# Optimization experiments

Hardware: AMD Instinct MI355X
Metric: run time of the kernel (lower is better)

The kernel has to match this reference:

```python
import jax, jax.numpy as jnp
import numpy as np
from jax import lax

R = 4                 # radius (init kwarg)
EPS = 2.0             # eps (init kwarg)
K = 2 * R + 1         # stencil size


def _dir_kernels():
    """8 directional box kernels [8,1,K,K]: L,R,U,D,NW,NE,SW,SE (matches torch construction)."""
    base = np.ones((K, K), np.float32)
    L = base.copy(); L[:, R + 1:] = 0
    Rk = base.copy(); Rk[:, :R] = 0
    U = base.copy(); U[R + 1:, :] = 0
    D = base.copy(); D[:R, :] = 0
    NW = U.copy(); NE = U.copy(); SW = D.copy(); SE = D.copy()
    half = float((R + 1) * (2 * R + 1))
    L, Rk, U, D = L / half, Rk / half, U / half, D / half
    NW[:, R + 1:] = 0; NE[:, :R] = 0; SW[:, R + 1:] = 0; SE[:, :R] = 0
    quad = float((R + 1) ** 2)
    NW, NE, SW, SE = NW / quad, NE / quad, SW / quad, SE / quad
    return jnp.asarray(np.stack([L, Rk, U, D, NW, NE, SW, SE])[:, None])


def _pad(x):
    # ReplicationPad2d(R)
    return jnp.pad(x, ((0, 0), (0, 0), (R, R), (R, R)), mode='edge')


def _conv(x, w, groups=1):
    return lax.conv_general_dilated(
        x, w, window_strides=(1, 1), padding='VALID',
        dimension_numbers=('NCHW', 'OIHW', 'NCHW'), feature_group_count=groups)


def _resize_bilinear_ac(x, H, W):
    """Bilinear resize with align_corners=True, separable gather. x: [N,C,h,w]."""
    n, c, h, w = x.shape
    dt = x.dtype

    def coords(out, src):
        t = jnp.arange(out, dtype=dt) * (jnp.asarray(src - 1, dt) / jnp.asarray(out - 1, dt))
        i0 = jnp.clip(jnp.floor(t).astype(jnp.int32), 0, src - 2)
        f = t - i0.astype(dt)
        return i0, f

    y0, fy = coords(H, h)
    x0, fx = coords(W, w)
    rows = x[:, :, y0, :] * (1 - fy)[None, None, :, None] + x[:, :, y0 + 1, :] * fy[None, None, :, None]
    return rows[:, :, :, x0] * (1 - fx) + rows[:, :, :, x0 + 1] * fx


def setup_inputs() -> dict:
    key = jax.random.key(0)
    k1, k2, k3 = jax.random.split(key, 3)
    lr_x = jax.random.uniform(k1, (1, 3, 256, 256), jnp.float32) * 255.0
    lr_y = jax.random.uniform(k2, (1, 3, 256, 256), jnp.float32) * 255.0
    hr_x = jax.random.uniform(k3, (1, 3, 1024, 1024), jnp.float32) * 255.0
    box_w = jnp.full((3, 1, K, K), 1.0 / (K * K), jnp.float32)  # depthwise box filter weights
    return {"lr_x": lr_x, "lr_y": lr_y, "hr_x": hr_x, "box_w": box_w}


def reference(lr_x, lr_y, hr_x, box_w):
    H, W = hr_x.shape[2], hr_x.shape[3]
    box = lambda t: _conv(_pad(t), box_w, groups=3)

    # --- guided filter coefficients at low res ---
    mean_x = box(lr_x)
    mean_y = box(lr_y)
    cov_xy = box(lr_x * lr_y) - mean_x * mean_y
    var_x = box(lr_x * lr_x) - mean_x * mean_x
    A = cov_xy / (var_x + EPS)
    b = mean_y - A * mean_x

    # --- upsample A, b to hr (bilinear, align_corners=True) ---
    A = _resize_bilinear_ac(A, H, W)
    b = _resize_bilinear_ac(b, H, W)

    # --- 8-direction side-window stencil; channels treated as batch ---
    dirw = _dir_kernels()                      # [8,1,K,K]
    A3 = _pad(A.reshape(3, 1, H, W))
    b3 = _pad(b.reshape(3, 1, H, W))
    im3 = hr_x.reshape(3, 1, H, W)
    cA = _conv(A3, dirw)                       # [3,8,H,W]
    cB = _conv(b3, dirw)                       # [3,8,H,W]
    d = cA * im3 + cB - im3                    # [3,8,H,W]

    idx = jnp.argmin(jnp.abs(d), axis=1, keepdims=True)
    dm = jnp.take_along_axis(d, idx, axis=1)   # min-|delta| direction
    res = (dm + im3).reshape(1, 3, H, W)

    # res.int() truncates toward zero, then clamp(0,255), then float
    return jnp.clip(jnp.trunc(res), 0.0, 255.0)
```

## Files before the change

kernel.cpp:

```cpp
#include <hip/hip_runtime.h>

#define RR 4
#define LRN 256
#define HRN 1024
#define SCALE (255.0f/1023.0f)

#define LTW 32
#define LTH 8
#define LGW (LTW + 2*RR)
#define LGH (LTH + 2*RR)

#define TX 32
#define TYR 64
#define BTH 8
#define NROW (TYR / BTH)
#define LRC 12
#define LRR 20

__global__ __launch_bounds__(256) void lowres_coeffs(
    const float* __restrict__ lrx, const float* __restrict__ lry,
    float2* __restrict__ AB)
{
    __shared__ float4 sV[LGH][LGW];
    __shared__ float4 sH[LGH][LTW];

    const int c  = blockIdx.z;
    const int X0 = blockIdx.x * LTW, Y0 = blockIdx.y * LTH;
    const int tid = threadIdx.y * LTW + threadIdx.x;
    const float* px = lrx + c * LRN * LRN;
    const float* py = lry + c * LRN * LRN;

    for (int i = tid; i < LGH * LGW; i += 256) {
        int r = i / LGW, col = i - r * LGW;
        int gy = min(max(Y0 - RR + r, 0), LRN - 1);
        int gx = min(max(X0 - RR + col, 0), LRN - 1);
        float xv = px[gy * LRN + gx];
        float yv = py[gy * LRN + gx];
        sV[r][col] = make_float4(xv, yv, xv * yv, xv * xv);
    }
    __syncthreads();

    for (int i = tid; i < LGH * LTW; i += 256) {
        int r = i / LTW, col = i - r * LTW;
        float4 s = sV[r][col];
        #pragma unroll
        for (int k = 1; k < 9; ++k) {
            float4 v = sV[r][col + k];
            s.x += v.x; s.y += v.y; s.z += v.z; s.w += v.w;
        }
        sH[r][col] = s;
    }
    __syncthreads();

    const int tx = threadIdx.x, ty = threadIdx.y;
    float4 s = sH[ty][tx];
    #pragma unroll
    for (int k = 1; k < 9; ++k) {
        float4 v = sH[ty + k][tx];
        s.x += v.x; s.y += v.y; s.z += v.z; s.w += v.w;
    }
    const float inv81 = 1.0f / 81.0f;
    float mx = s.x * inv81, my = s.y * inv81;
    float cov = s.z * inv81 - mx * my;
    float var = s.w * inv81 - mx * mx;
    float A = cov / (var + 2.0f);
    float B = my - A * mx;
    AB[(c * LRN + Y0 + ty) * LRN + X0 + tx] = make_float2(A, B);
}

__device__ inline int anchor_of(int u) {
    int k = min(max(u - 4, 0), HRN - 1);
    float t = (float)k * SCALE;
    int i = (int)t; if (i > LRN - 2) i = LRN - 2;
    return i;
}

__device__ inline float4 mkw(int k0, int k1, int a) {
    float4 w = make_float4(0.f, 0.f, 0.f, 0.f);
    for (int k = k0; k <= k1; ++k) {
        int kc = min(max(k, 0), HRN - 1);
        float t = (float)kc * SCALE;
        int i = (int)t; if (i > LRN - 2) i = LRN - 2;
        float f = t - (float)i;
        int off = i - a;
        float wa = 1.0f - f, wb = f;
        w.x += (off == 0) ? wa : 0.0f;
        w.y += (off == 1) ? wa : ((off == 0) ? wb : 0.0f);
        w.z += (off == 2) ? wa : ((off == 1) ? wb : 0.0f);
        w.w += (off == 2) ? wb : 0.0f;
    }
    return w;
}

__global__ __launch_bounds__(256, 6) void stencil_kernel(
    const float2* __restrict__ AB,
    const float* __restrict__ hrx, float* __restrict__ out)
{
    __shared__ float2 sAB[LRR][LRC];
    __shared__ float2 sT[TYR][LRC];
    __shared__ float2 sB[TYR][LRC];
    __shared__ float2 sF[TYR][LRC];
    __shared__ float4 sYW[TYR][3];
    __shared__ int    sYA[TYR];
    __shared__ float4 sXW[TX][3];
    __shared__ int    sXA[TX];

    const int c  = blockIdx.z;
    const int X0 = blockIdx.x * TX, Y0 = blockIdx.y * TYR;
    const int tid = threadIdx.y * TX + threadIdx.x;
    const float2* ABc = AB + c * LRN * LRN;

    const int rowbase = anchor_of(Y0);
    const int colbase = anchor_of(X0);

    if (tid < TX) {
        int x = X0 + tid;
        int a = anchor_of(x);
        sXA[tid] = a - colbase;
        sXW[tid][0] = mkw(x - 4, x,     a);
        sXW[tid][1] = mkw(x,     x + 4, a);
        sXW[tid][2] = mkw(x - 4, x + 4, a);
    } else if (tid >= 64 && tid < 64 + TYR) {
        int r = tid - 64;
        int y = Y0 + r;
        int a = anchor_of(y);
        sYA[r] = a - rowbase;
        sYW[r][0] = mkw(y - 4, y,     a);
        sYW[r][1] = mkw(y,     y + 4, a);
        sYW[r][2] = mkw(y - 4, y + 4, a);
    }
    for (int i = tid; i < LRR * LRC; i += 256) {
        int r = i / LRC, cc = i - r * LRC;
        int gr = min(rowbase + r, LRN - 1);
        int gc = min(colbase + cc, LRN - 1);
        sAB[r][cc] = ABc[gr * LRN + gc];
    }
    __syncthreads();

    for (int i = tid; i < TYR * LRC; i += 256) {
        int r = i / LRC, cc = i - r * LRC;
        int ra = sYA[r];
        float4 wT = sYW[r][0], wB = sYW[r][1], wF = sYW[r][2];
        float2 v0 = sAB[ra][cc],     v1 = sAB[ra + 1][cc];
        float2 v2 = sAB[ra + 2][cc], v3 = sAB[ra + 3][cc];
        sT[r][cc] = make_float2(wT.x*v0.x + wT.y*v1.x + wT.z*v2.x + wT.w*v3.x,
                                wT.x*v0.y + wT.y*v1.y + wT.z*v2.y + wT.w*v3.y);
        sB[r][cc] = make_float2(wB.x*v0.x + wB.y*v1.x + wB.z*v2.x + wB.w*v3.x,
                                wB.x*v0.y + wB.y*v1.y + wB.z*v2.y + wB.w*v3.y);
        sF[r][cc] = make_float2(wF.x*v0.x + wF.y*v1.x + wF.z*v2.x + wF.w*v3.x,
                                wF.x*v0.y + wF.y*v1.y + wF.z*v2.y + wF.w*v3.y);
    }
    __syncthreads();

    const int tx = threadIdx.x, tyw = threadIdx.y;
    const int c0 = sXA[tx];
    const float4 wL = sXW[tx][0], wR = sXW[tx][1], wFh = sXW[tx][2];
    const float i45 = 1.0f / 45.0f, i25 = 1.0f / 25.0f;
    const float* hp = hrx + (c * HRN + Y0 + tyw) * HRN + X0 + tx;
    float*       op = out + (c * HRN + Y0 + tyw) * HRN + X0 + tx;

    #pragma unroll
    for (int j = 0; j < NROW; ++j) {
        const int r = tyw + j * BTH;
        float LA=0,Lb=0, RA=0,Rb=0, UA=0,Ub=0, DA=0,Db=0;
        float NWA=0,NWb=0, NEA=0,NEb=0, SWA=0,SWb=0, SEA=0,SEb=0;
        #pragma unroll
        for (int k = 0; k < 4; ++k) {
            float wl = (k==0)?wL.x:(k==1)?wL.y:(k==2)?wL.z:wL.w;
            float wr = (k==0)?wR.x:(k==1)?wR.y:(k==2)?wR.z:wR.w;
            float wf = (k==0)?wFh.x:(k==1)?wFh.y:(k==2)?wFh.z:wFh.w;
            float2 tv = sT[r][c0 + k];
            float2 bv = sB[r][c0 + k];
            float2 fv = sF[r][c0 + k];
            LA = fmaf(wl, fv.x, LA);   Lb = fmaf(wl, fv.y, Lb);
            RA = fmaf(wr, fv.x, RA);   Rb = fmaf(wr, fv.y, Rb);
            UA = fmaf(wf, tv.x, UA);   Ub = fmaf(wf, tv.y, Ub);
            DA = fmaf(wf, bv.x, DA);   Db = fmaf(wf, bv.y, Db);
            NWA = fmaf(wl, tv.x, NWA); NWb = fmaf(wl, tv.y, NWb);
            NEA = fmaf(wr, tv.x, NEA); NEb = fmaf(wr, tv.y, NEb);
            SWA = fmaf(wl, bv.x, SWA); SWb = fmaf(wl, bv.y, SWb);
            SEA = fmaf(wr, bv.x, SEA); SEb = fmaf(wr, bv.y, SEb);
        }
        float xv = hp[j * BTH * HRN];

        float d0 = fmaf(i45, fmaf(LA,  xv, Lb),  -xv);
        float d1 = fmaf(i45, fmaf(RA,  xv, Rb),  -xv);
        float d2 = fmaf(i45, fmaf(UA,  xv, Ub),  -xv);
        float d3 = fmaf(i45, fmaf(DA,  xv, Db),  -xv);
        float d4 = fmaf(i25, fmaf(NWA, xv, NWb), -xv);
        float d5 = fmaf(i25, fmaf(NEA, xv, NEb), -xv);
        float d6 = fmaf(i25, fmaf(SWA, xv, SWb), -xv);
        float d7 = fmaf(i25, fmaf(SEA, xv, SEb), -xv);

        float a0 = fabsf(d0), a1 = fabsf(d1), a2 = fabsf(d2), a3 = fabsf(d3);
        float a4 = fabsf(d4), a5 = fabsf(d5), a6 = fabsf(d6), a7 = fabsf(d7);
        bool c01 = a0 <= a1; float w01 = c01 ? d0 : d1; float m01 = c01 ? a0 : a1;
        bool c23 = a2 <= a3; float w23 = c23 ? d2 : d3; float m23 = c23 ? a2 : a3;
        bool c45 = a4 <= a5; float w45 = c45 ? d4 : d5; float m45 = c45 ? a4 : a5;
        bool c67 = a6 <= a7; float w67 = c67 ? d6 : d7; float m67 = c67 ? a6 : a7;
        bool cA_ = m01 <= m23; float wA = cA_ ? w01 : w23; float mA = cA_ ? m01 : m23;
        bool cB_ = m45 <= m67; float wB_ = cB_ ? w45 : w67; float mB = cB_ ? m45 : m67;
        float bd = (mA <= mB) ? wA : wB_;

        float res = __builtin_amdgcn_fmed3f(truncf(bd + xv), 0.0f, 255.0f);
        op[j * BTH * HRN] = res;
    }
}

extern "C" void kernel_launch(void* const* d_in, const int* in_sizes, int n_in,
                              void* d_out, int out_size, void* d_ws, size_t ws_size,
                              hipStream_t stream) {
    const float* lrx = (const float*)d_in[0];
    const float* lry = (const float*)d_in[1];
    const float* hrx = (const float*)d_in[2];
    (void)d_in[3]; (void)in_sizes; (void)n_in; (void)out_size; (void)ws_size;

    float2* AB = (float2*)d_ws;
    float* outp = (float*)d_out;

    dim3 lblock(LTW, LTH);
    dim3 lgrid(LRN / LTW, LRN / LTH, 3);
    lowres_coeffs<<<lgrid, lblock, 0, stream>>>(lrx, lry, AB);

    dim3 sblock(TX, BTH);
    dim3 sgrid(HRN / TX, HRN / TYR, 3);
    stencil_kernel<<<sgrid, sblock, 0, stream>>>(AB, hrx, outp);
}
```

Before: 87.74 us.

## Fuse low-res guided-filter coefficient computation into the high-res stencil kernel

Removes the separate low-res coefficient kernel and its global A/B workspace; each stencil block now recomputes the box-filtered A,b for its own low-res halo tile in shared memory, reusing one shared region for both the box sums and the row-interpolated buffers. Inner accumulations are rewritten with 2-wide vector FMAs so the compiler can emit packed FP32 math. This saves one kernel launch and a global round-trip, but adds redundant halo work per block and a larger shared footprint that may reduce occupancy.

After: 85.23 us. -2.9%, faster.

```diff
diff --git a/kernel.cpp b/kernel.cpp
--- a/kernel.cpp
+++ b/kernel.cpp
@@ -4,11 +4,6 @@
 #define LRN 256
 #define HRN 1024
 #define SCALE (255.0f/1023.0f)
-
-#define LTW 32
-#define LTH 8
-#define LGW (LTW + 2*RR)
-#define LGH (LTH + 2*RR)
 
 #define TX 32
 #define TYR 64
@@ -16,57 +11,10 @@
 #define NROW (TYR / BTH)
 #define LRC 12
 #define LRR 20
-
-__global__ __launch_bounds__(256) void lowres_coeffs(
-    const float* __restrict__ lrx, const float* __restrict__ lry,
-    float2* __restrict__ AB)
-{
-    __shared__ float4 sV[LGH][LGW];
-    __shared__ float4 sH[LGH][LTW];
-
-    const int c  = blockIdx.z;
-    const int X0 = blockIdx.x * LTW, Y0 = blockIdx.y * LTH;
-    const int tid = threadIdx.y * LTW + threadIdx.x;
-    const float* px = lrx + c * LRN * LRN;
-    const float* py = lry + c * LRN * LRN;
-
-    for (int i = tid; i < LGH * LGW; i += 256) {
-        int r = i / LGW, col = i - r * LGW;
-        int gy = min(max(Y0 - RR + r, 0), LRN - 1);
-        int gx = min(max(X0 - RR + col, 0), LRN - 1);
-        float xv = px[gy * LRN + gx];
-        float yv = py[gy * LRN + gx];
-        sV[r][col] = make_float4(xv, yv, xv * yv, xv * xv);
-    }
-    __syncthreads();
-
-    for (int i = tid; i < LGH * LTW; i += 256) {
-        int r = i / LTW, col = i - r * LTW;
-        float4 s = sV[r][col];
-        #pragma unroll
-        for (int k = 1; k < 9; ++k) {
-            float4 v = sV[r][col + k];
-            s.x += v.x; s.y += v.y; s.z += v.z; s.w += v.w;
-        }
-        sH[r][col] = s;
-    }
-    __syncthreads();
-
-    const int tx = threadIdx.x, ty = threadIdx.y;
-    float4 s = sH[ty][tx];
-    #pragma unroll
-    for (int k = 1; k < 9; ++k) {
-        float4 v = sH[ty + k][tx];
-        s.x += v.x; s.y += v.y; s.z += v.z; s.w += v.w;
-    }
-    const float inv81 = 1.0f / 81.0f;
-    float mx = s.x * inv81, my = s.y * inv81;
-    float cov = s.z * inv81 - mx * my;
-    float var = s.w * inv81 - mx * mx;
-    float A = cov / (var + 2.0f);
-    float B = my - A * mx;
-    AB[(c * LRN + Y0 + ty) * LRN + X0 + tx] = make_float2(A, B);
-}
+#define GC (LRC + 8)
+#define GR (LRR + 8)
+
+typedef float v2 __attribute__((ext_vector_type(2)));
 
 __device__ inline int anchor_of(int u) {
     int k = min(max(u - 4, 0), HRN - 1);
@@ -92,14 +40,18 @@
     return w;
 }
 
-__global__ __launch_bounds__(256, 6) void stencil_kernel(
-    const float2* __restrict__ AB,
+__global__ __launch_bounds__(256, 6) void fused_kernel(
+    const float* __restrict__ lrx, const float* __restrict__ lry,
     const float* __restrict__ hrx, float* __restrict__ out)
 {
-    __shared__ float2 sAB[LRR][LRC];
-    __shared__ float2 sT[TYR][LRC];
-    __shared__ float2 sB[TYR][LRC];
-    __shared__ float2 sF[TYR][LRC];
+    __shared__ alignas(16) char region1[18432];
+    float4 (*sV)[GC]  = reinterpret_cast<float4(*)[GC]>(region1);
+    float4 (*sHS)[LRC] = reinterpret_cast<float4(*)[LRC]>(region1 + GR * GC * 16);
+    v2 (*sT)[LRC]  = reinterpret_cast<v2(*)[LRC]>(region1);
+    v2 (*sBm)[LRC] = reinterpret_cast<v2(*)[LRC]>(region1 + 6144);
+    v2 (*sF)[LRC]  = reinterpret_cast<v2(*)[LRC]>(region1 + 12288);
+
+    __shared__ v2     sAB[LRR][LRC];
     __shared__ float4 sYW[TYR][3];
     __shared__ int    sYA[TYR];
     __shared__ float4 sXW[TX][3];
@@ -108,7 +60,8 @@
     const int c  = blockIdx.z;
     const int X0 = blockIdx.x * TX, Y0 = blockIdx.y * TYR;
     const int tid = threadIdx.y * TX + threadIdx.x;
-    const float2* ABc = AB + c * LRN * LRN;
+    const float* px = lrx + c * LRN * LRN;
+    const float* py = lry + c * LRN * LRN;
 
     const int rowbase = anchor_of(Y0);
     const int colbase = anchor_of(X0);
@@ -129,11 +82,45 @@
         sYW[r][1] = mkw(y,     y + 4, a);
         sYW[r][2] = mkw(y - 4, y + 4, a);
     }
+
+    for (int i = tid; i < GR * GC; i += 256) {
+        int r = i / GC, cc = i - r * GC;
+        int gy = min(max(rowbase - 4 + r, 0), LRN - 1);
+        int gx = min(max(colbase - 4 + cc, 0), LRN - 1);
+        float xv = px[gy * LRN + gx];
+        float yv = py[gy * LRN + gx];
+        sV[r][cc] = make_float4(xv, yv, xv * yv, xv * xv);
+    }
+    __syncthreads();
+
+    for (int i = tid; i < GR * LRC; i += 256) {
+        int r = i / LRC, cc = i - r * LRC;
+        float4 s = sV[r][cc];
+        #pragma unroll
+        for (int k = 1; k < 9; ++k) {
+            float4 v = sV[r][cc + k];
+            s.x += v.x; s.y += v.y; s.z += v.z; s.w += v.w;
+        }
+        sHS[r][cc] = s;
+    }
+    __syncthreads();
+
     for (int i = tid; i < LRR * LRC; i += 256) {
         int r = i / LRC, cc = i - r * LRC;
-        int gr = min(rowbase + r, LRN - 1);
-        int gc = min(colbase + cc, LRN - 1);
-        sAB[r][cc] = ABc[gr * LRN + gc];
+        float4 s = sHS[r][cc];
+        #pragma unroll
+        for (int k = 1; k < 9; ++k) {
+            float4 v = sHS[r + k][cc];
+            s.x += v.x; s.y += v.y; s.z += v.z; s.w += v.w;
+        }
+        const float inv81 = 1.0f / 81.0f;
+        float mx = s.x * inv81, my = s.y * inv81;
+        float cov = s.z * inv81 - mx * my;
+        float var = s.w * inv81 - mx * mx;
+        float A = cov / (var + 2.0f);
+        float B = my - A * mx;
+        v2 ab; ab.x = A; ab.y = B;
+        sAB[r][cc] = ab;
     }
     __syncthreads();
 
@@ -141,14 +128,19 @@
         int r = i / LRC, cc = i - r * LRC;
         int ra = sYA[r];
         float4 wT = sYW[r][0], wB = sYW[r][1], wF = sYW[r][2];
-        float2 v0 = sAB[ra][cc],     v1 = sAB[ra + 1][cc];
-        float2 v2 = sAB[ra + 2][cc], v3 = sAB[ra + 3][cc];
-        sT[r][cc] = make_float2(wT.x*v0.x + wT.y*v1.x + wT.z*v2.x + wT.w*v3.x,
-                                wT.x*v0.y + wT.y*v1.y + wT.z*v2.y + wT.w*v3.y);
-        sB[r][cc] = make_float2(wB.x*v0.x + wB.y*v1.x + wB.z*v2.x + wB.w*v3.x,
-                                wB.x*v0.y + wB.y*v1.y + wB.z*v2.y + wB.w*v3.y);
-        sF[r][cc] = make_float2(wF.x*v0.x + wF.y*v1.x + wF.z*v2.x + wF.w*v3.x,
-                                wF.x*v0.y + wF.y*v1.y + wF.z*v2.y + wF.w*v3.y);
+        v2 v0 = sAB[ra][cc],     v1 = sAB[ra + 1][cc];
+        v2 v2_ = sAB[ra + 2][cc], v3 = sAB[ra + 3][cc];
+        v2 t, b, f;
+        t = v0 * wT.x; t = __builtin_elementwise_fma((v2)(wT.y), v1, t);
+        t = __builtin_elementwise_fma((v2)(wT.z), v2_, t);
+        t = __builtin_elementwise_fma((v2)(wT.w), v3, t);
+        b = v0 * wB.x; b = __builtin_elementwise_fma((v2)(wB.y), v1, b);
+        b = __builtin_elementwise_fma((v2)(wB.z), v2_, b);
+        b = __builtin_elementwise_fma((v2)(wB.w), v3, b);
+        f = v0 * wF.x; f = __builtin_elementwise_fma((v2)(wF.y), v1, f);
+        f = __builtin_elementwise_fma((v2)(wF.z), v2_, f);
+        f = __builtin_elementwise_fma((v2)(wF.w), v3, f);
+        sT[r][cc] = t; sBm[r][cc] = b; sF[r][cc] = f;
     }
     __syncthreads();
 
@@ -162,35 +154,35 @@
     #pragma unroll
     for (int j = 0; j < NROW; ++j) {
         const int r = tyw + j * BTH;
-        float LA=0,Lb=0, RA=0,Rb=0, UA=0,Ub=0, DA=0,Db=0;
-        float NWA=0,NWb=0, NEA=0,NEb=0, SWA=0,SWb=0, SEA=0,SEb=0;
+        v2 aL = 0, aR = 0, aU = 0, aD = 0;
+        v2 aNW = 0, aNE = 0, aSW = 0, aSE = 0;
         #pragma unroll
         for (int k = 0; k < 4; ++k) {
             float wl = (k==0)?wL.x:(k==1)?wL.y:(k==2)?wL.z:wL.w;
             float wr = (k==0)?wR.x:(k==1)?wR.y:(k==2)?wR.z:wR.w;
             float wf = (k==0)?wFh.x:(k==1)?wFh.y:(k==2)?wFh.z:wFh.w;
-            float2 tv = sT[r][c0 + k];
-            float2 bv = sB[r][c0 + k];
-            float2 fv = sF[r][c0 + k];
-            LA = fmaf(wl, fv.x, LA);   Lb = fmaf(wl, fv.y, Lb);
-            RA = fmaf(wr, fv.x, RA);   Rb = fmaf(wr, fv.y, Rb);
-            UA = fmaf(wf, tv.x, UA);   Ub = fmaf(wf, tv.y, Ub);
-            DA = fmaf(wf, bv.x, DA);   Db = fmaf(wf, bv.y, Db);
-            NWA = fmaf(wl, tv.x, NWA); NWb = fmaf(wl, tv.y, NWb);
-            NEA = fmaf(wr, tv.x, NEA); NEb = fmaf(wr, tv.y, NEb);
-            SWA = fmaf(wl, bv.x, SWA); SWb = fmaf(wl, bv.y, SWb);
-            SEA = fmaf(wr, bv.x, SEA); SEb = fmaf(wr, bv.y, SEb);
+            v2 tv = sT[r][c0 + k];
+            v2 bv = sBm[r][c0 + k];
+            v2 fv = sF[r][c0 + k];
+            aL  = __builtin_elementwise_fma((v2)(wl), fv, aL);
+            aR  = __builtin_elementwise_fma((v2)(wr), fv, aR);
+            aU  = __builtin_elementwise_fma((v2)(wf), tv, aU);
+            aD  = __builtin_elementwise_fma((v2)(wf), bv, aD);
+            aNW = __builtin_elementwise_fma((v2)(wl), tv, aNW);
+            aNE = __builtin_elementwise_fma((v2)(wr), tv, aNE);
+            aSW = __builtin_elementwise_fma((v2)(wl), bv, aSW);
+            aSE = __builtin_elementwise_fma((v2)(wr), bv, aSE);
         }
         float xv = hp[j * BTH * HRN];
 
-        float d0 = fmaf(i45, fmaf(LA,  xv, Lb),  -xv);
-        float d1 = fmaf(i45, fmaf(RA,  xv, Rb),  -xv);
-        float d2 = fmaf(i45, fmaf(UA,  xv, Ub),  -xv);
-        float d3 = fmaf(i45, fmaf(DA,  xv, Db),  -xv);
-        float d4 = fmaf(i25, fmaf(NWA, xv, NWb), -xv);
-        float d5 = fmaf(i25, fmaf(NEA, xv, NEb), -xv);
-        float d6 = fmaf(i25, fmaf(SWA, xv, SWb), -xv);
-        float d7 = fmaf(i25, fmaf(SEA, xv, SEb), -xv);
+        float d0 = fmaf(i45, fmaf(aL.x,  xv, aL.y),  -xv);
+        float d1 = fmaf(i45, fmaf(aR.x,  xv, aR.y),  -xv);
+        float d2 = fmaf(i45, fmaf(aU.x,  xv, aU.y),  -xv);
+        float d3 = fmaf(i45, fmaf(aD.x,  xv, aD.y),  -xv);
+        float d4 = fmaf(i25, fmaf(aNW.x, xv, aNW.y), -xv);
+        float d5 = fmaf(i25, fmaf(aNE.x, xv, aNE.y), -xv);
+        float d6 = fmaf(i25, fmaf(aSW.x, xv, aSW.y), -xv);
+        float d7 = fmaf(i25, fmaf(aSE.x, xv, aSE.y), -xv);
 
         float a0 = fabsf(d0), a1 = fabsf(d1), a2 = fabsf(d2), a3 = fabsf(d3);
         float a4 = fabsf(d4), a5 = fabsf(d5), a6 = fabsf(d6), a7 = fabsf(d7);
@@ -213,16 +205,11 @@
     const float* lrx = (const float*)d_in[0];
     const float* lry = (const float*)d_in[1];
     const float* hrx = (const float*)d_in[2];
-    (void)d_in[3]; (void)in_sizes; (void)n_in; (void)out_size; (void)ws_size;
-
-    float2* AB = (float2*)d_ws;
+    (void)d_in[3]; (void)in_sizes; (void)n_in; (void)out_size;
+    (void)d_ws; (void)ws_size;
+
     float* outp = (float*)d_out;
-
-    dim3 lblock(LTW, LTH);
-    dim3 lgrid(LRN / LTW, LRN / LTH, 3);
-    lowres_coeffs<<<lgrid, lblock, 0, stream>>>(lrx, lry, AB);
-
-    dim3 sblock(TX, BTH);
-    dim3 sgrid(HRN / TX, HRN / TYR, 3);
-    stencil_kernel<<<sgrid, sblock, 0, stream>>>(AB, hrx, outp);
-}
+    dim3 block(TX, BTH);
+    dim3 grid(HRN / TX, HRN / TYR, 3);
+    fused_kernel<<<grid, block, 0, stream>>>(lrx, lry, hrx, outp);
+}
```
